# Kernel tuning notes

Measured on AMD Instinct MI355X. Metric: run time of the kernel, lower is better.

Reference implementation:

```python
import jax, jax.numpy as jnp
import numpy as np

B, S, IN_DIM, EMBED, H = 2, 2048, 512, 512, 8
HD = EMBED // H


def setup_inputs() -> dict:
    key = jax.random.key(0)
    ks = jax.random.split(key, 6)
    x = jax.random.normal(ks[0], (B, S, IN_DIM), dtype=jnp.float32)
    dist_mat = jax.random.normal(ks[1], (B, H, S, S), dtype=jnp.float32) * 0.02
    path_mat = jax.random.normal(ks[2], (B, H, S, S), dtype=jnp.float32) * 0.02
    # xavier-uniform-style init scale
    qkv_w = jax.random.normal(ks[3], (IN_DIM, 3 * EMBED), dtype=jnp.float32) * (1.0 / np.sqrt(IN_DIM))
    qkv_b = jnp.zeros((3 * EMBED,), dtype=jnp.float32)
    o_w = jax.random.normal(ks[4], (EMBED, EMBED), dtype=jnp.float32) * (1.0 / np.sqrt(EMBED))
    o_b = jnp.zeros((EMBED,), dtype=jnp.float32)
    return {"x": x, "dist_mat": dist_mat, "path_mat": path_mat,
            "qkv_w": qkv_w, "qkv_b": qkv_b, "o_w": o_w, "o_b": o_b}


def reference(x, dist_mat, path_mat, qkv_w, qkv_b, o_w, o_b):
    b, s, _ = x.shape
    qkv = x @ qkv_w + qkv_b                         # [B,S,3*EMBED]
    qkv = qkv.reshape(b, s, H, 3 * HD).transpose(0, 2, 1, 3)  # [B,H,S,3*HD]
    q, k, v = jnp.split(qkv, 3, axis=-1)            # each [B,H,S,HD]
    logits = jnp.einsum('bhqd,bhkd->bhqk', q, k) / jnp.sqrt(jnp.float32(HD))
    attn = jax.nn.softmax(logits, axis=-1)
    attn = attn + dist_mat + path_mat               # post-softmax bias (breaks flash fusion)
    vals = jnp.einsum('bhqk,bhkd->bhqd', attn, v)   # [B,H,S,HD]
    vals = vals.transpose(0, 2, 1, 3).reshape(b, s, EMBED)
    return vals @ o_w + o_b
```

## Files before the change

### kernel.cpp

```cpp
#include <hip/hip_runtime.h>
#include <stdint.h>
#include <stddef.h>

#define B_ 2
#define H_ 8
#define S_ 2048
#define D_ 64
#define E_ 512
#define N3_ 1536
#define M_ (B_*S_)
#define K_ 512

typedef __attribute__((ext_vector_type(4))) float f32x4;
typedef __attribute__((ext_vector_type(8))) __bf16 bf16x8;
typedef __attribute__((ext_vector_type(4))) __bf16 bf16x4;

static __device__ __forceinline__ int swz(int b) { return b ^ (((b >> 7) & 7) << 4); }

static __device__ __forceinline__ void gl_lds16(const void* g, void* l) {
    __builtin_amdgcn_global_load_lds((const __attribute__((address_space(1))) void*)g,
                                     (__attribute__((address_space(3))) void*)l, 16, 0, 0);
}

__global__ void cvt_bf16_kernel(const float* __restrict__ in, __bf16* __restrict__ out, int n4) {
    int i = blockIdx.x * blockDim.x + threadIdx.x;
    if (i < n4) {
        float4 v = reinterpret_cast<const float4*>(in)[i];
        bf16x4 o;
        o[0] = (__bf16)v.x; o[1] = (__bf16)v.y; o[2] = (__bf16)v.z; o[3] = (__bf16)v.w;
        reinterpret_cast<bf16x4*>(out)[i] = o;
    }
}

__global__ void transpose_cvt_kernel(const float* __restrict__ in, __bf16* __restrict__ out,
                                     int R, int C) {
    __shared__ float tile[32][33];
    int tc = blockIdx.x * 32, tr = blockIdx.y * 32;
    int lx = threadIdx.x & 31, ly = threadIdx.x >> 5;
    #pragma unroll
    for (int p = 0; p < 4; ++p) {
        int r = tr + ly + p * 8, c = tc + lx;
        if (r < R && c < C) tile[ly + p * 8][lx] = in[(size_t)r * C + c];
    }
    __syncthreads();
    #pragma unroll
    for (int p = 0; p < 4; ++p) {
        int oc = tc + ly + p * 8;
        int orow = tr + lx;
        if (oc < C && orow < R) out[(size_t)oc * R + orow] = (__bf16)tile[lx][ly + p * 8];
    }
}

__global__ void transpose_v_kernel(const __bf16* __restrict__ v, __bf16* __restrict__ vt) {
    __shared__ __bf16 t[64][65];
    int bh = blockIdx.x >> 5;
    int s0 = (blockIdx.x & 31) << 6;
    int tid = threadIdx.x;
    const __bf16* src = v + ((size_t)bh * S_ + s0) * D_;
    #pragma unroll
    for (int p = 0; p < 2; ++p) {
        int idx = (p * 256 + tid) * 8;
        int r = idx >> 6, c = idx & 63;
        bf16x8 val = *reinterpret_cast<const bf16x8*>(src + (size_t)r * D_ + c);
        #pragma unroll
        for (int e = 0; e < 8; ++e) t[r][c + e] = val[e];
    }
    __syncthreads();
    __bf16* dst = vt + (size_t)bh * D_ * S_ + s0;
    #pragma unroll
    for (int p = 0; p < 16; ++p) {
        int idx = p * 256 + tid;
        int d = idx >> 6, s = idx & 63;
        dst[(size_t)d * S_ + s] = t[s][d];
    }
}

template<int MODE>
__global__ __launch_bounds__(256, 2) void gemm_kernel(
    const __bf16* __restrict__ A, const __bf16* __restrict__ Bt,
    const float* __restrict__ bias,
    void* __restrict__ o0, void* __restrict__ o1, void* __restrict__ o2,
    int M, int N, int K)
{
    __shared__ __align__(16) __bf16 lA[128 * 64];
    __shared__ __align__(16) __bf16 lB[128 * 64];
    const int tid = threadIdx.x;
    const int wave = tid >> 6, lane = tid & 63;
    const int wm = wave >> 1, wn = wave & 1;
    const int m0 = blockIdx.y * 128, n0 = blockIdx.x * 128;
    const int l15 = lane & 15, l4 = lane >> 4;

    f32x4 acc[4][4] = {};

    for (int k0 = 0; k0 < K; k0 += 64) {
        __syncthreads();
        #pragma unroll
        for (int p = 0; p < 4; ++p) {
            int base = p * 4096 + wave * 1024;
            int js = swz(base + lane * 16);
            int row = js >> 7, colb = js & 127;
            gl_lds16((const char*)A + ((size_t)(m0 + row) * K + k0) * 2 + colb, (char*)lA + base);
            gl_lds16((const char*)Bt + ((size_t)(n0 + row) * K + k0) * 2 + colb, (char*)lB + base);
        }
        __syncthreads();
        #pragma unroll
        for (int ks = 0; ks < 2; ++ks) {
            bf16x8 af[4], bfr[4];
            #pragma unroll
            for (int i = 0; i < 4; ++i) {
                af[i]  = *(const bf16x8*)((const char*)lA + swz(((wm * 64 + i * 16 + l15) << 7) + ks * 64 + (l4 << 4)));
                bfr[i] = *(const bf16x8*)((const char*)lB + swz(((wn * 64 + i * 16 + l15) << 7) + ks * 64 + (l4 << 4)));
            }
            #pragma unroll
            for (int i = 0; i < 4; ++i)
                #pragma unroll
                for (int j = 0; j < 4; ++j)
                    acc[i][j] = __builtin_amdgcn_mfma_f32_16x16x32_bf16(af[i], bfr[j], acc[i][j], 0, 0, 0);
        }
    }
    #pragma unroll
    for (int i = 0; i < 4; ++i) {
        int mg0 = m0 + wm * 64 + i * 16 + (l4 << 2);
        #pragma unroll
        for (int j = 0; j < 4; ++j) {
            int ng = n0 + wn * 64 + j * 16 + l15;
            float bv = bias[ng];
            #pragma unroll
            for (int r = 0; r < 4; ++r) {
                int m = mg0 + r;
                float val = acc[i][j][r] + bv;
                if (MODE == 0) {
                    int h = ng / 192, rr = ng % 192;
                    int which = rr >> 6, d = rr & 63;
                    int b = m >> 11, s = m & (S_ - 1);
                    if (which == 0) val *= 0.125f;
                    __bf16* dst = which == 0 ? (__bf16*)o0 : which == 1 ? (__bf16*)o1 : (__bf16*)o2;
                    dst[(((size_t)((b * H_ + h) * S_ + s)) << 6) + d] = (__bf16)val;
                } else {
                    ((float*)o0)[(size_t)m * N + ng] = val;
                }
            }
        }
    }
}

__global__ __launch_bounds__(256, 2) void attn_kernel(
    const __bf16* __restrict__ q, const __bf16* __restrict__ k,
    const __bf16* __restrict__ vt,
    const float* __restrict__ dist, const float* __restrict__ path,
    __bf16* __restrict__ vals)
{
    __shared__ __align__(16) __bf16 kl[2][64 * 64];
    __shared__ __align__(16) __bf16 vl[2][64 * 64];
    __shared__ __align__(16) __bf16 pl[4][16 * 64];
    const int tid = threadIdx.x, wave = tid >> 6, lane = tid & 63;
    const int l15 = lane & 15, l4 = lane >> 4;
    const int id = blockIdx.x;
    const int xcd = id & 7, j = id >> 3;
    const int bh = xcd * 2 + (j >> 5);
    const int q0 = (j & 31) << 6;
    const int b = bh >> 3, h = bh & 7;
    const int qrow = q0 + wave * 16 + l15;

    const __bf16* qp = q + ((size_t)bh * S_ + qrow) * D_;
    bf16x8 qf0 = *(const bf16x8*)(qp + (l4 << 3));
    bf16x8 qf1 = *(const bf16x8*)(qp + 32 + (l4 << 3));

    const float* dp = dist + ((size_t)bh * S_ + qrow) * S_;
    const float* pp = path + ((size_t)bh * S_ + qrow) * S_;

    const char* kg = (const char*)(k + (size_t)bh * S_ * D_);
    const char* vg = (const char*)(vt + (size_t)bh * D_ * S_);

    auto STAGE = [&](int kt, int buf) {
        #pragma unroll
        for (int p = 0; p < 2; ++p) {
            int base = p * 4096 + wave * 1024;
            int js = swz(base + lane * 16);
            int row = js >> 7, colb = js & 127;
            gl_lds16(kg + ((size_t)(kt + row) * D_) * 2 + colb, (char*)kl[buf] + base);
            gl_lds16(vg + ((size_t)row * S_ + kt) * 2 + colb, (char*)vl[buf] + base);
        }
    };
    float4 fb[8];
    auto BLOAD = [&](int kt) {
        #pragma unroll
        for (int ks = 0; ks < 2; ++ks) {
            int kc = kt + ks * 32 + (l4 << 3);
            fb[ks * 2 + 0] = *(const float4*)(dp + kc);
            fb[ks * 2 + 1] = *(const float4*)(dp + kc + 4);
            fb[4 + ks * 2 + 0] = *(const float4*)(pp + kc);
            fb[4 + ks * 2 + 1] = *(const float4*)(pp + kc + 4);
        }
    };

    float m_run[4], l_run[4];
    f32x4 o_p[4] = {}, o_b[4] = {};
    #pragma unroll
    for (int r = 0; r < 4; ++r) { m_run[r] = -1e30f; l_run[r] = 0.f; }

    STAGE(0, 0);
    BLOAD(0);
    __syncthreads();

    int cur = 0;
    for (int kt = 0; kt < S_; kt += 64) {
        bf16x8 ba[2];
        #pragma unroll
        for (int ks = 0; ks < 2; ++ks) {
            float4 d0 = fb[ks * 2], d1 = fb[ks * 2 + 1];
            float4 p0 = fb[4 + ks * 2], p1 = fb[4 + ks * 2 + 1];
            ba[ks][0] = (__bf16)(d0.x + p0.x); ba[ks][1] = (__bf16)(d0.y + p0.y);
            ba[ks][2] = (__bf16)(d0.z + p0.z); ba[ks][3] = (__bf16)(d0.w + p0.w);
            ba[ks][4] = (__bf16)(d1.x + p1.x); ba[ks][5] = (__bf16)(d1.y + p1.y);
            ba[ks][6] = (__bf16)(d1.z + p1.z); ba[ks][7] = (__bf16)(d1.w + p1.w);
        }
        int ktn = (kt + 64 < S_) ? kt + 64 : kt;
        STAGE(ktn, cur ^ 1);
        BLOAD(ktn);

        f32x4 lg[4] = {};
        #pragma unroll
        for (int ks = 0; ks < 2; ++ks) {
            bf16x8 qa = ks ? qf1 : qf0;
            #pragma unroll
            for (int n = 0; n < 4; ++n) {
                bf16x8 kf = *(const bf16x8*)((const char*)kl[cur] + swz(((n * 16 + l15) << 7) + ks * 64 + (l4 << 4)));
                lg[n] = __builtin_amdgcn_mfma_f32_16x16x32_bf16(qa, kf, lg[n], 0, 0, 0);
            }
        }
        #pragma unroll
        for (int ks = 0; ks < 2; ++ks)
            #pragma unroll
            for (int n = 0; n < 4; ++n) {
                bf16x8 vf = *(const bf16x8*)((const char*)vl[cur] + swz(((n * 16 + l15) << 7) + ks * 64 + (l4 << 4)));
                o_b[n] = __builtin_amdgcn_mfma_f32_16x16x32_bf16(ba[ks], vf, o_b[n], 0, 0, 0);
            }
        float scale[4], rsum[4], pe[4][4];
        #pragma unroll
        for (int r = 0; r < 4; ++r) {
            float t = fmaxf(fmaxf(lg[0][r], lg[1][r]), fmaxf(lg[2][r], lg[3][r]));
            t = fmaxf(t, __shfl_xor(t, 1));
            t = fmaxf(t, __shfl_xor(t, 2));
            t = fmaxf(t, __shfl_xor(t, 4));
            t = fmaxf(t, __shfl_xor(t, 8));
            float mnew = fmaxf(m_run[r], t);
            scale[r] = __expf(m_run[r] - mnew);
            m_run[r] = mnew;
            rsum[r] = 0.f;
        }
        #pragma unroll
        for (int n = 0; n < 4; ++n)
            #pragma unroll
            for (int r = 0; r < 4; ++r) {
                pe[n][r] = __expf(lg[n][r] - m_run[r]);
                rsum[r] += pe[n][r];
            }
        #pragma unroll
        for (int r = 0; r < 4; ++r) {
            float s = rsum[r];
            s += __shfl_xor(s, 1);
            s += __shfl_xor(s, 2);
            s += __shfl_xor(s, 4);
            s += __shfl_xor(s, 8);
            l_run[r] = l_run[r] * scale[r] + s;
        }
        #pragma unroll
        for (int n = 0; n < 4; ++n)
            #pragma unroll
            for (int r = 0; r < 4; ++r)
                o_p[n][r] *= scale[r];
        char* pb = (char*)&pl[wave][0];
        #pragma unroll
        for (int n = 0; n < 4; ++n)
            #pragma unroll
            for (int r = 0; r < 4; ++r) {
                int prow = (l4 << 2) + r, pcol = n * 16 + l15;
                *(__bf16*)(pb + swz((prow << 7) + pcol * 2)) = (__bf16)pe[n][r];
            }
        #pragma unroll
        for (int ks = 0; ks < 2; ++ks) {
            bf16x8 pa = *(const bf16x8*)((const char*)pb + swz((l15 << 7) + ks * 64 + (l4 << 4)));
            #pragma unroll
            for (int n = 0; n < 4; ++n) {
                bf16x8 vf = *(const bf16x8*)((const char*)vl[cur] + swz(((n * 16 + l15) << 7) + ks * 64 + (l4 << 4)));
                o_p[n] = __builtin_amdgcn_mfma_f32_16x16x32_bf16(pa, vf, o_p[n], 0, 0, 0);
            }
        }
        __syncthreads();
        cur ^= 1;
    }
    #pragma unroll
    for (int r = 0; r < 4; ++r) {
        int s = q0 + wave * 16 + (l4 << 2) + r;
        float inv = 1.f / l_run[r];
        __bf16* dst = vals + (size_t)(b * S_ + s) * E_ + h * D_;
        #pragma unroll
        for (int n = 0; n < 4; ++n) {
            int d = n * 16 + l15;
            dst[d] = (__bf16)(o_p[n][r] * inv + o_b[n][r]);
        }
    }
}

extern "C" void kernel_launch(void* const* d_in, const int* in_sizes, int n_in,
                              void* d_out, int out_size, void* d_ws, size_t ws_size,
                              hipStream_t stream) {
    (void)in_sizes; (void)n_in; (void)out_size; (void)ws_size;
    const float* x      = (const float*)d_in[0];
    const float* dist   = (const float*)d_in[1];
    const float* path   = (const float*)d_in[2];
    const float* qkv_w  = (const float*)d_in[3];
    const float* qkv_b  = (const float*)d_in[4];
    const float* o_w    = (const float*)d_in[5];
    const float* o_b    = (const float*)d_in[6];
    float* out = (float*)d_out;

    char* ws = (char*)d_ws;
    __bf16* xb     = (__bf16*)(ws);
    __bf16* qkv_wT = (__bf16*)(ws + (4  << 20));
    __bf16* o_wT   = (__bf16*)(ws + (6  << 20));
    __bf16* qb     = (__bf16*)(ws + (7  << 20));
    __bf16* kb     = (__bf16*)(ws + (11 << 20));
    __bf16* vb     = (__bf16*)(ws + (15 << 20));
    __bf16* vtb    = (__bf16*)(ws + (19 << 20));
    __bf16* valsb  = (__bf16*)(ws + (23 << 20));

    cvt_bf16_kernel<<<(M_ * K_ / 4 + 255) / 256, 256, 0, stream>>>(x, xb, M_ * K_ / 4);
    transpose_cvt_kernel<<<dim3(N3_ / 32, K_ / 32), 256, 0, stream>>>(qkv_w, qkv_wT, K_, N3_);
    transpose_cvt_kernel<<<dim3(E_ / 32, E_ / 32), 256, 0, stream>>>(o_w, o_wT, E_, E_);
    gemm_kernel<0><<<dim3(N3_ / 128, M_ / 128), 256, 0, stream>>>(xb, qkv_wT, qkv_b, qb, kb, vb, M_, N3_, K_);
    transpose_v_kernel<<<B_ * H_ * (S_ / 64), 256, 0, stream>>>(vb, vtb);
    attn_kernel<<<B_ * H_ * (S_ / 64), 256, 0, stream>>>(qb, kb, vtb, dist, path, valsb);
    gemm_kernel<1><<<dim3(E_ / 128, M_ / 128), 256, 0, stream>>>(valsb, o_wT, o_b, out, nullptr, nullptr, M_, E_, K_);
}
```

Measured before the change: 192.6 us.

## Use single-wave attention blocks reading K/V directly from global memory

Restructures the attention kernel so each block is one 64-thread wave handling 16 query rows, launching four times as many blocks. The shared-memory double-buffered K/V staging and block barriers are removed, and each wave loads its K and V fragments straight from global memory (relying on L2/cache reuse). The o_b MFMA is also merged into the P·V loop. This removes synchronization and LDS traffic, at the cost of four times the K/V global reads per head and higher register use.

```diff
diff --git a/kernel.cpp b/kernel.cpp
--- a/kernel.cpp
+++ b/kernel.cpp
@@ -144,23 +144,21 @@
     }
 }
 
-__global__ __launch_bounds__(256, 2) void attn_kernel(
+__global__ __launch_bounds__(64, 2) void attn_kernel(
     const __bf16* __restrict__ q, const __bf16* __restrict__ k,
     const __bf16* __restrict__ vt,
     const float* __restrict__ dist, const float* __restrict__ path,
     __bf16* __restrict__ vals)
 {
-    __shared__ __align__(16) __bf16 kl[2][64 * 64];
-    __shared__ __align__(16) __bf16 vl[2][64 * 64];
-    __shared__ __align__(16) __bf16 pl[4][16 * 64];
-    const int tid = threadIdx.x, wave = tid >> 6, lane = tid & 63;
+    __shared__ __align__(16) __bf16 pl[16 * 64];
+    const int lane = threadIdx.x;
     const int l15 = lane & 15, l4 = lane >> 4;
     const int id = blockIdx.x;
     const int xcd = id & 7, j = id >> 3;
-    const int bh = xcd * 2 + (j >> 5);
-    const int q0 = (j & 31) << 6;
+    const int bh = xcd * 2 + (j >> 7);
+    const int q0 = (j & 127) << 4;
     const int b = bh >> 3, h = bh & 7;
-    const int qrow = q0 + wave * 16 + l15;
+    const int qrow = q0 + l15;
 
     const __bf16* qp = q + ((size_t)bh * S_ + qrow) * D_;
     bf16x8 qf0 = *(const bf16x8*)(qp + (l4 << 3));
@@ -168,20 +166,9 @@
 
     const float* dp = dist + ((size_t)bh * S_ + qrow) * S_;
     const float* pp = path + ((size_t)bh * S_ + qrow) * S_;
-
     const char* kg = (const char*)(k + (size_t)bh * S_ * D_);
     const char* vg = (const char*)(vt + (size_t)bh * D_ * S_);
 
-    auto STAGE = [&](int kt, int buf) {
-        #pragma unroll
-        for (int p = 0; p < 2; ++p) {
-            int base = p * 4096 + wave * 1024;
-            int js = swz(base + lane * 16);
-            int row = js >> 7, colb = js & 127;
-            gl_lds16(kg + ((size_t)(kt + row) * D_) * 2 + colb, (char*)kl[buf] + base);
-            gl_lds16(vg + ((size_t)row * S_ + kt) * 2 + colb, (char*)vl[buf] + base);
-        }
-    };
     float4 fb[8];
     auto BLOAD = [&](int kt) {
         #pragma unroll
@@ -199,11 +186,9 @@
     #pragma unroll
     for (int r = 0; r < 4; ++r) { m_run[r] = -1e30f; l_run[r] = 0.f; }
 
-    STAGE(0, 0);
     BLOAD(0);
-    __syncthreads();
-
-    int cur = 0;
+
+    #pragma unroll 1
     for (int kt = 0; kt < S_; kt += 64) {
         bf16x8 ba[2];
         #pragma unroll
@@ -216,26 +201,25 @@
             ba[ks][6] = (__bf16)(d1.z + p1.z); ba[ks][7] = (__bf16)(d1.w + p1.w);
         }
         int ktn = (kt + 64 < S_) ? kt + 64 : kt;
-        STAGE(ktn, cur ^ 1);
         BLOAD(ktn);
 
+        bf16x8 kf[2][4], vf[2][4];
+        #pragma unroll
+        for (int ks = 0; ks < 2; ++ks)
+            #pragma unroll
+            for (int n = 0; n < 4; ++n) {
+                kf[ks][n] = *(const bf16x8*)(kg + (size_t)(kt + n * 16 + l15) * 128 + ks * 64 + (l4 << 4));
+                vf[ks][n] = *(const bf16x8*)(vg + (size_t)(n * 16 + l15) * (S_ * 2) + kt * 2 + ks * 64 + (l4 << 4));
+            }
+
         f32x4 lg[4] = {};
         #pragma unroll
         for (int ks = 0; ks < 2; ++ks) {
             bf16x8 qa = ks ? qf1 : qf0;
             #pragma unroll
-            for (int n = 0; n < 4; ++n) {
-                bf16x8 kf = *(const bf16x8*)((const char*)kl[cur] + swz(((n * 16 + l15) << 7) + ks * 64 + (l4 << 4)));
-                lg[n] = __builtin_amdgcn_mfma_f32_16x16x32_bf16(qa, kf, lg[n], 0, 0, 0);
-            }
-        }
-        #pragma unroll
-        for (int ks = 0; ks < 2; ++ks)
-            #pragma unroll
-            for (int n = 0; n < 4; ++n) {
-                bf16x8 vf = *(const bf16x8*)((const char*)vl[cur] + swz(((n * 16 + l15) << 7) + ks * 64 + (l4 << 4)));
-                o_b[n] = __builtin_amdgcn_mfma_f32_16x16x32_bf16(ba[ks], vf, o_b[n], 0, 0, 0);
-            }
+            for (int n = 0; n < 4; ++n)
+                lg[n] = __builtin_amdgcn_mfma_f32_16x16x32_bf16(qa, kf[ks][n], lg[n], 0, 0, 0);
+        }
         float scale[4], rsum[4], pe[4][4];
         #pragma unroll
         for (int r = 0; r < 4; ++r) {
@@ -270,7 +254,7 @@
             #pragma unroll
             for (int r = 0; r < 4; ++r)
                 o_p[n][r] *= scale[r];
-        char* pb = (char*)&pl[wave][0];
+        char* pb = (char*)pl;
         #pragma unroll
         for (int n = 0; n < 4; ++n)
             #pragma unroll
@@ -283,16 +267,14 @@
             bf16x8 pa = *(const bf16x8*)((const char*)pb + swz((l15 << 7) + ks * 64 + (l4 << 4)));
             #pragma unroll
             for (int n = 0; n < 4; ++n) {
-                bf16x8 vf = *(const bf16x8*)((const char*)vl[cur] + swz(((n * 16 + l15) << 7) + ks * 64 + (l4 << 4)));
-                o_p[n] = __builtin_amdgcn_mfma_f32_16x16x32_bf16(pa, vf, o_p[n], 0, 0, 0);
-            }
-        }
-        __syncthreads();
-        cur ^= 1;
+                o_p[n] = __builtin_amdgcn_mfma_f32_16x16x32_bf16(pa, vf[ks][n], o_p[n], 0, 0, 0);
+                o_b[n] = __builtin_amdgcn_mfma_f32_16x16x32_bf16(ba[ks], vf[ks][n], o_b[n], 0, 0, 0);
+            }
+        }
     }
     #pragma unroll
     for (int r = 0; r < 4; ++r) {
-        int s = q0 + wave * 16 + (l4 << 2) + r;
+        int s = q0 + (l4 << 2) + r;
         float inv = 1.f / l_run[r];
         __bf16* dst = vals + (size_t)(b * S_ + s) * E_ + h * D_;
         #pragma unroll
@@ -331,6 +313,6 @@
     transpose_cvt_kernel<<<dim3(E_ / 32, E_ / 32), 256, 0, stream>>>(o_w, o_wT, E_, E_);
     gemm_kernel<0><<<dim3(N3_ / 128, M_ / 128), 256, 0, stream>>>(xb, qkv_wT, qkv_b, qb, kb, vb, M_, N3_, K_);
     transpose_v_kernel<<<B_ * H_ * (S_ / 64), 256, 0, stream>>>(vb, vtb);
-    attn_kernel<<<B_ * H_ * (S_ / 64), 256, 0, stream>>>(qb, kb, vtb, dist, path, valsb);
+    attn_kernel<<<B_ * H_ * (S_ / 16), 64, 0, stream>>>(qb, kb, vtb, dist, path, valsb);
     gemm_kernel<1><<<dim3(E_ / 128, M_ / 128), 256, 0, stream>>>(valsb, o_wT, o_b, out, nullptr, nullptr, M_, E_, K_);
 }
```

Result: slower. 261.2 us (+35.6%).

## Split attention key dimension in two with a combine kernel

Applied to the files above, without the earlier changes.

The attention kernel now splits the key range into two halves (split-K, flash-decoding style), doubling the grid to 1024 blocks. Each block writes its partial normalized attention output, its bias-weighted output and its running max and sum, and a new combine kernel merges the halves with log-sum-exp weights before the output projection. Launch bounds go from 2 to 4 blocks per CU to raise occupancy. This adds a kernel launch and partial-result traffic through global memory in exchange for more parallelism across the GPU, and the tighter launch bound risks register spills.

```diff
diff --git a/kernel.cpp b/kernel.cpp
--- a/kernel.cpp
+++ b/kernel.cpp
@@ -144,11 +144,12 @@
     }
 }
 
-__global__ __launch_bounds__(256, 2) void attn_kernel(
+__global__ __launch_bounds__(256, 4) void attn_kernel(
     const __bf16* __restrict__ q, const __bf16* __restrict__ k,
     const __bf16* __restrict__ vt,
     const float* __restrict__ dist, const float* __restrict__ path,
-    __bf16* __restrict__ vals)
+    __bf16* __restrict__ attno, __bf16* __restrict__ biaso,
+    float* __restrict__ ml)
 {
     __shared__ __align__(16) __bf16 kl[2][64 * 64];
     __shared__ __align__(16) __bf16 vl[2][64 * 64];
@@ -157,9 +158,11 @@
     const int l15 = lane & 15, l4 = lane >> 4;
     const int id = blockIdx.x;
     const int xcd = id & 7, j = id >> 3;
-    const int bh = xcd * 2 + (j >> 5);
-    const int q0 = (j & 31) << 6;
-    const int b = bh >> 3, h = bh & 7;
+    const int bh = xcd * 2 + (j >> 6);
+    const int r2 = j & 63;
+    const int ksid = r2 >> 5;
+    const int q0 = (r2 & 31) << 6;
+    const int kbase = ksid << 10;
     const int qrow = q0 + wave * 16 + l15;
 
     const __bf16* qp = q + ((size_t)bh * S_ + qrow) * D_;
@@ -168,7 +171,6 @@
 
     const float* dp = dist + ((size_t)bh * S_ + qrow) * S_;
     const float* pp = path + ((size_t)bh * S_ + qrow) * S_;
-
     const char* kg = (const char*)(k + (size_t)bh * S_ * D_);
     const char* vg = (const char*)(vt + (size_t)bh * D_ * S_);
 
@@ -199,12 +201,14 @@
     #pragma unroll
     for (int r = 0; r < 4; ++r) { m_run[r] = -1e30f; l_run[r] = 0.f; }
 
-    STAGE(0, 0);
-    BLOAD(0);
+    STAGE(kbase, 0);
+    BLOAD(kbase);
     __syncthreads();
 
     int cur = 0;
-    for (int kt = 0; kt < S_; kt += 64) {
+    #pragma unroll 1
+    for (int it = 0; it < 16; ++it) {
+        int kt = kbase + it * 64;
         bf16x8 ba[2];
         #pragma unroll
         for (int ks = 0; ks < 2; ++ks) {
@@ -215,7 +219,7 @@
             ba[ks][4] = (__bf16)(d1.x + p1.x); ba[ks][5] = (__bf16)(d1.y + p1.y);
             ba[ks][6] = (__bf16)(d1.z + p1.z); ba[ks][7] = (__bf16)(d1.w + p1.w);
         }
-        int ktn = (kt + 64 < S_) ? kt + 64 : kt;
+        int ktn = (it < 15) ? kt + 64 : kt;
         STAGE(ktn, cur ^ 1);
         BLOAD(ktn);
 
@@ -293,14 +297,44 @@
     #pragma unroll
     for (int r = 0; r < 4; ++r) {
         int s = q0 + wave * 16 + (l4 << 2) + r;
+        size_t rowi = (size_t)(ksid * 16 + bh) * S_ + s;
         float inv = 1.f / l_run[r];
-        __bf16* dst = vals + (size_t)(b * S_ + s) * E_ + h * D_;
         #pragma unroll
         for (int n = 0; n < 4; ++n) {
             int d = n * 16 + l15;
-            dst[d] = (__bf16)(o_p[n][r] * inv + o_b[n][r]);
-        }
-    }
+            attno[rowi * D_ + d] = (__bf16)(o_p[n][r] * inv);
+            biaso[rowi * D_ + d] = (__bf16)o_b[n][r];
+        }
+        if (l15 == 0) {
+            ml[rowi * 2 + 0] = m_run[r];
+            ml[rowi * 2 + 1] = l_run[r];
+        }
+    }
+}
+
+__global__ void combine_kernel(const __bf16* __restrict__ attno, const __bf16* __restrict__ biaso,
+                               const float* __restrict__ ml, __bf16* __restrict__ out) {
+    int i = blockIdx.x * blockDim.x + threadIdx.x;
+    int row = i >> 3;
+    int d0 = (i & 7) * 8;
+    int bh = row >> 11, s = row & (S_ - 1);
+    const int half = 16 * S_;
+    float m0 = ml[(size_t)row * 2], l0 = ml[(size_t)row * 2 + 1];
+    float m1 = ml[(size_t)(half + row) * 2], l1 = ml[(size_t)(half + row) * 2 + 1];
+    float m = fmaxf(m0, m1);
+    float w0 = __expf(m0 - m) * l0, w1 = __expf(m1 - m) * l1;
+    float inv = 1.f / (w0 + w1);
+    w0 *= inv; w1 *= inv;
+    bf16x8 a0 = *(const bf16x8*)(attno + (size_t)row * D_ + d0);
+    bf16x8 a1 = *(const bf16x8*)(attno + (size_t)(half + row) * D_ + d0);
+    bf16x8 b0 = *(const bf16x8*)(biaso + (size_t)row * D_ + d0);
+    bf16x8 b1 = *(const bf16x8*)(biaso + (size_t)(half + row) * D_ + d0);
+    bf16x8 o;
+    #pragma unroll
+    for (int e = 0; e < 8; ++e)
+        o[e] = (__bf16)(w0 * (float)a0[e] + w1 * (float)a1[e] + (float)b0[e] + (float)b1[e]);
+    int b = bh >> 3, h = bh & 7;
+    *(bf16x8*)(out + ((size_t)(b * S_ + s) * E_) + h * D_ + d0) = o;
 }
 
 extern "C" void kernel_launch(void* const* d_in, const int* in_sizes, int n_in,
@@ -318,19 +352,23 @@
 
     char* ws = (char*)d_ws;
     __bf16* xb     = (__bf16*)(ws);
+    __bf16* valsb  = (__bf16*)(ws);
     __bf16* qkv_wT = (__bf16*)(ws + (4  << 20));
-    __bf16* o_wT   = (__bf16*)(ws + (6  << 20));
-    __bf16* qb     = (__bf16*)(ws + (7  << 20));
-    __bf16* kb     = (__bf16*)(ws + (11 << 20));
-    __bf16* vb     = (__bf16*)(ws + (15 << 20));
-    __bf16* vtb    = (__bf16*)(ws + (19 << 20));
-    __bf16* valsb  = (__bf16*)(ws + (23 << 20));
+    __bf16* o_wT   = (__bf16*)(ws + (4  << 20) + (3 << 19));
+    __bf16* qb     = (__bf16*)(ws + (6  << 20));
+    __bf16* kb     = (__bf16*)(ws + (10 << 20));
+    __bf16* vtb    = (__bf16*)(ws + (14 << 20));
+    __bf16* vb     = (__bf16*)(ws + (18 << 20));
+    __bf16* attno  = (__bf16*)(ws + (18 << 20));
+    __bf16* biaso  = (__bf16*)(ws + (26 << 20));
+    float*  ml     = (float*) (ws + (34 << 20));
 
     cvt_bf16_kernel<<<(M_ * K_ / 4 + 255) / 256, 256, 0, stream>>>(x, xb, M_ * K_ / 4);
     transpose_cvt_kernel<<<dim3(N3_ / 32, K_ / 32), 256, 0, stream>>>(qkv_w, qkv_wT, K_, N3_);
     transpose_cvt_kernel<<<dim3(E_ / 32, E_ / 32), 256, 0, stream>>>(o_w, o_wT, E_, E_);
     gemm_kernel<0><<<dim3(N3_ / 128, M_ / 128), 256, 0, stream>>>(xb, qkv_wT, qkv_b, qb, kb, vb, M_, N3_, K_);
     transpose_v_kernel<<<B_ * H_ * (S_ / 64), 256, 0, stream>>>(vb, vtb);
-    attn_kernel<<<B_ * H_ * (S_ / 64), 256, 0, stream>>>(qb, kb, vtb, dist, path, valsb);
+    attn_kernel<<<1024, 256, 0, stream>>>(qb, kb, vtb, dist, path, attno, biaso, ml);
+    combine_kernel<<<1024, 256, 0, stream>>>(attno, biaso, ml, valsb);
     gemm_kernel<1><<<dim3(E_ / 128, M_ / 128), 256, 0, stream>>>(valsb, o_wT, o_b, out, nullptr, nullptr, M_, E_, K_);
 }
```

Result: no change. 194.9 us (+1.2%).

## Stage dist/path bias tiles through LDS with async global_load_lds

Applied to the files above, without the earlier changes.

Replaces the per-thread register prefetch of the dist and path bias rows with asynchronous global-to-LDS copies. These go into a double-buffered, XOR-swizzled LDS tile that is staged together with K and V. Each wave then reads its bias fragments from LDS and sums them in fp32 before converting to bf16 for the MFMA. Launch bounds drop to one block per CU because of the larger shared-memory footprint, which lowers occupancy in exchange for fewer live registers and more overlap of the bias stream with compute.

```diff
diff --git a/kernel.cpp b/kernel.cpp
--- a/kernel.cpp
+++ b/kernel.cpp
@@ -144,7 +144,7 @@
     }
 }
 
-__global__ __launch_bounds__(256, 2) void attn_kernel(
+__global__ __launch_bounds__(256, 1) void attn_kernel(
     const __bf16* __restrict__ q, const __bf16* __restrict__ k,
     const __bf16* __restrict__ vt,
     const float* __restrict__ dist, const float* __restrict__ path,
@@ -153,6 +153,7 @@
     __shared__ __align__(16) __bf16 kl[2][64 * 64];
     __shared__ __align__(16) __bf16 vl[2][64 * 64];
     __shared__ __align__(16) __bf16 pl[4][16 * 64];
+    __shared__ __align__(16) float  bl[2][2][4][1024];
     const int tid = threadIdx.x, wave = tid >> 6, lane = tid & 63;
     const int l15 = lane & 15, l4 = lane >> 4;
     const int id = blockIdx.x;
@@ -166,9 +167,8 @@
     bf16x8 qf0 = *(const bf16x8*)(qp + (l4 << 3));
     bf16x8 qf1 = *(const bf16x8*)(qp + 32 + (l4 << 3));
 
-    const float* dp = dist + ((size_t)bh * S_ + qrow) * S_;
-    const float* pp = path + ((size_t)bh * S_ + qrow) * S_;
-
+    const char* dg = (const char*)(dist + (size_t)bh * S_ * S_);
+    const char* pg = (const char*)(path + (size_t)bh * S_ * S_);
     const char* kg = (const char*)(k + (size_t)bh * S_ * D_);
     const char* vg = (const char*)(vt + (size_t)bh * D_ * S_);
 
@@ -181,16 +181,14 @@
             gl_lds16(kg + ((size_t)(kt + row) * D_) * 2 + colb, (char*)kl[buf] + base);
             gl_lds16(vg + ((size_t)row * S_ + kt) * 2 + colb, (char*)vl[buf] + base);
         }
-    };
-    float4 fb[8];
-    auto BLOAD = [&](int kt) {
-        #pragma unroll
-        for (int ks = 0; ks < 2; ++ks) {
-            int kc = kt + ks * 32 + (l4 << 3);
-            fb[ks * 2 + 0] = *(const float4*)(dp + kc);
-            fb[ks * 2 + 1] = *(const float4*)(dp + kc + 4);
-            fb[4 + ks * 2 + 0] = *(const float4*)(pp + kc);
-            fb[4 + ks * 2 + 1] = *(const float4*)(pp + kc + 4);
+        #pragma unroll
+        for (int p = 0; p < 4; ++p) {
+            int jj = p * 64 + lane;
+            int row = jj >> 4;
+            int csrc = (jj & 15) ^ (row & 7);
+            size_t goff = ((size_t)(q0 + wave * 16 + row) * S_ + kt) * 4 + csrc * 16;
+            gl_lds16(dg + goff, (char*)&bl[buf][0][wave][0] + jj * 16);
+            gl_lds16(pg + goff, (char*)&bl[buf][1][wave][0] + jj * 16);
         }
     };
 
@@ -200,24 +198,34 @@
     for (int r = 0; r < 4; ++r) { m_run[r] = -1e30f; l_run[r] = 0.f; }
 
     STAGE(0, 0);
-    BLOAD(0);
     __syncthreads();
 
     int cur = 0;
+    #pragma unroll 1
     for (int kt = 0; kt < S_; kt += 64) {
-        bf16x8 ba[2];
-        #pragma unroll
-        for (int ks = 0; ks < 2; ++ks) {
-            float4 d0 = fb[ks * 2], d1 = fb[ks * 2 + 1];
-            float4 p0 = fb[4 + ks * 2], p1 = fb[4 + ks * 2 + 1];
-            ba[ks][0] = (__bf16)(d0.x + p0.x); ba[ks][1] = (__bf16)(d0.y + p0.y);
-            ba[ks][2] = (__bf16)(d0.z + p0.z); ba[ks][3] = (__bf16)(d0.w + p0.w);
-            ba[ks][4] = (__bf16)(d1.x + p1.x); ba[ks][5] = (__bf16)(d1.y + p1.y);
-            ba[ks][6] = (__bf16)(d1.z + p1.z); ba[ks][7] = (__bf16)(d1.w + p1.w);
-        }
         int ktn = (kt + 64 < S_) ? kt + 64 : kt;
         STAGE(ktn, cur ^ 1);
-        BLOAD(ktn);
+        __builtin_amdgcn_sched_barrier(0);
+
+        bf16x8 ba[2];
+        {
+            const char* dl = (const char*)&bl[cur][0][wave][0];
+            const char* plp = (const char*)&bl[cur][1][wave][0];
+            #pragma unroll
+            for (int ks = 0; ks < 2; ++ks) {
+                int c0 = ks * 8 + (l4 << 1);
+                int a0 = (l15 * 16 + (c0 ^ (l15 & 7))) * 16;
+                int a1 = (l15 * 16 + ((c0 + 1) ^ (l15 & 7))) * 16;
+                f32x4 d0 = *(const f32x4*)(dl + a0);
+                f32x4 d1 = *(const f32x4*)(dl + a1);
+                f32x4 p0 = *(const f32x4*)(plp + a0);
+                f32x4 p1 = *(const f32x4*)(plp + a1);
+                ba[ks][0] = (__bf16)(d0[0] + p0[0]); ba[ks][1] = (__bf16)(d0[1] + p0[1]);
+                ba[ks][2] = (__bf16)(d0[2] + p0[2]); ba[ks][3] = (__bf16)(d0[3] + p0[3]);
+                ba[ks][4] = (__bf16)(d1[0] + p1[0]); ba[ks][5] = (__bf16)(d1[1] + p1[1]);
+                ba[ks][6] = (__bf16)(d1[2] + p1[2]); ba[ks][7] = (__bf16)(d1[3] + p1[3]);
+            }
+        }
 
         f32x4 lg[4] = {};
         #pragma unroll
```

New measurement: 211.5 us. +9.8%, slower.
